# Performance work log

Hardware: AMD Instinct MI355X
Metric: run time of the kernel (lower is better)

The kernel has to match this reference:

```python
import jax, jax.numpy as jnp
import numpy as np

HID = 2048      # hidden_size
NH = 32         # num_heads
G = 8           # num_kv_groups
R = NH // G     # repeat factor (heads per kv group)
HD = HID // NH  # head_dim = 64
SCALE = HD ** 0.5


def setup_inputs() -> dict:
    key = jax.random.key(0)
    ks = jax.random.split(key, 10)
    B, S = 2, 1024
    x = jax.random.normal(ks[0], (B, S, HID), dtype=jnp.float32)
    attention_mask = jnp.ones((B, S, S), dtype=jnp.float32)
    # Linear params stored as [in, out] (y = x @ W + b), same math as torch Linear.
    Wq = jax.random.normal(ks[1], (HID, HID), dtype=jnp.float32) * 0.02
    bq = jnp.zeros((HID,), dtype=jnp.float32)
    Wk = jax.random.normal(ks[2], (HID, G * HD), dtype=jnp.float32) * 0.02
    bk = jnp.zeros((G * HD,), dtype=jnp.float32)
    Wv = jax.random.normal(ks[3], (HID, G * HD), dtype=jnp.float32) * 0.02
    bv = jnp.zeros((G * HD,), dtype=jnp.float32)
    Wo = jax.random.normal(ks[4], (HID, HID), dtype=jnp.float32) * 0.02
    bo = jnp.zeros((HID,), dtype=jnp.float32)
    return {"x": x, "attention_mask": attention_mask,
            "Wq": Wq, "bq": bq, "Wk": Wk, "bk": bk,
            "Wv": Wv, "bv": bv, "Wo": Wo, "bo": bo}


def reference(x, attention_mask, Wq, bq, Wk, bk, Wv, bv, Wo, bo):
    B, S, _ = x.shape
    # Projections. Group heads as (G, R) instead of repeat_interleave:
    # repeat_interleave(key, R, dim=2) duplicates each kv group R times, which is
    # exactly sharing key[:, :, g] across the R heads of group g.
    q = (x @ Wq + bq).reshape(B, S, G, R, HD)   # [B,S,G,R,HD] (heads = G*R in order)
    k = (x @ Wk + bk).reshape(B, S, G, HD)      # [B,S,G,HD]
    v = (x @ Wv + bv).reshape(B, S, G, HD)
    # scores [B,G,R,Sq,Sk] == torch's [B, NH, Sq, Sk] with NH = G*R
    scores = jnp.einsum('bqgrd,bkgd->bgrqk', q, k) / SCALE
    scores = scores * attention_mask[:, None, None]  # multiplicative mask per head
    w = jax.nn.softmax(scores, axis=-1)
    out = jnp.einsum('bgrqk,bkgd->bqgrd', w, v).reshape(B, S, HID)
    return out @ Wo + bo + x
```

## Files before the change

### kernel.cpp

```cpp
#include <hip/hip_runtime.h>

typedef unsigned short u16;
typedef unsigned int u32;
typedef __attribute__((ext_vector_type(8))) short bf16x8;
typedef __attribute__((ext_vector_type(4))) float f32x4;

#define HID 2048
#define S_LEN 1024
#define BATCH 2
#define G_KV 8
#define R_REP 4
#define HD 64
#define NQKV 3072

__device__ __forceinline__ u16 f2bf(float f) {
    union { u32 u; float ff; } x; x.ff = f;
    u32 u = x.u;
    u += 0x7FFFu + ((u >> 16) & 1u);
    return (u16)(u >> 16);
}

__device__ __forceinline__ void gload_lds16(const void* g, void* l) {
    __builtin_amdgcn_global_load_lds((const __attribute__((address_space(1))) void*)g,
                                     (__attribute__((address_space(3))) void*)l,
                                     16, 0, 0);
}

__global__ __launch_bounds__(256) void cvt_x(const float* __restrict__ in,
                                             u16* __restrict__ out) {
    int i = (blockIdx.x * 256 + threadIdx.x) * 8;
    float4 a = *(const float4*)(in + i);
    float4 b = *(const float4*)(in + i + 4);
    u16 t[8] = {f2bf(a.x), f2bf(a.y), f2bf(a.z), f2bf(a.w),
                f2bf(b.x), f2bf(b.y), f2bf(b.z), f2bf(b.w)};
    *(uint4*)(out + i) = *(const uint4*)t;
}

__global__ __launch_bounds__(256) void mask_perm(const float* __restrict__ mask,
                                                 float* __restrict__ out) {
    __shared__ float tile[64 * 68];
    int bid = blockIdx.x;
    int kt = bid & 15, qblk = (bid >> 4) & 15, b = bid >> 8;
    int t = threadIdx.x;
    int row = t >> 2, c0 = (t & 3) * 16;
    const float* src = mask + ((size_t)b * S_LEN + qblk * 64 + row) * S_LEN + kt * 64 + c0;
#pragma unroll
    for (int i = 0; i < 4; ++i)
        *(float4*)&tile[row * 68 + c0 + i * 4] = *(const float4*)(src + i * 4);
    __syncthreads();
    int w = t >> 6, quad = (t >> 4) & 3, l16 = t & 15;
    int q = w * 16 + l16;
    float* dst = out + (size_t)bid * 4096 + t * 16;
#pragma unroll
    for (int mt = 0; mt < 4; ++mt) {
        float4 v = *(const float4*)&tile[q * 68 + mt * 16 + quad * 4];
        *(float4*)(dst + mt * 4) = v;
    }
}

__global__ __launch_bounds__(256) void transpose_qkv(const float* __restrict__ Wq,
                                                     const float* __restrict__ Wk,
                                                     const float* __restrict__ Wv,
                                                     u16* __restrict__ out) {
    __shared__ float tile[32][33];
    int n0 = blockIdx.x * 32, k0 = blockIdx.y * 32;
    const float* in; int N, nc0;
    if (n0 < 2048)      { in = Wq; N = 2048; nc0 = n0; }
    else if (n0 < 2560) { in = Wk; N = 512;  nc0 = n0 - 2048; }
    else                { in = Wv; N = 512;  nc0 = n0 - 2560; }
    int tx = threadIdx.x, ty = threadIdx.y;
#pragma unroll
    for (int j = 0; j < 4; ++j)
        tile[ty + j * 8][tx] = in[(size_t)(k0 + ty + j * 8) * N + nc0 + tx];
    __syncthreads();
#pragma unroll
    for (int j = 0; j < 4; ++j)
        out[(size_t)(n0 + ty + j * 8) * 2048 + k0 + tx] = f2bf(tile[tx][ty + j * 8]);
}

__global__ __launch_bounds__(256) void transpose_cvt(const float* __restrict__ in,
                                                     u16* __restrict__ out,
                                                     int K, int N) {
    __shared__ float tile[32][33];
    int n0 = blockIdx.x * 32, k0 = blockIdx.y * 32;
    int tx = threadIdx.x, ty = threadIdx.y;
#pragma unroll
    for (int j = 0; j < 4; ++j)
        tile[ty + j * 8][tx] = in[(size_t)(k0 + ty + j * 8) * N + n0 + tx];
    __syncthreads();
#pragma unroll
    for (int j = 0; j < 4; ++j)
        out[(size_t)(n0 + ty + j * 8) * K + k0 + tx] = f2bf(tile[tx][ty + j * 8]);
}

__global__ __launch_bounds__(256) void gemm_qkv(const u16* __restrict__ Xb,
                                                const u16* __restrict__ WT,
                                                const float* __restrict__ bq,
                                                const float* __restrict__ bk,
                                                const float* __restrict__ bv,
                                                u16* __restrict__ qb,
                                                u16* __restrict__ kb,
                                                u16* __restrict__ vb) {
    __shared__ __align__(16) u16 As[64 * 32];
    __shared__ __align__(16) u16 Bs[128 * 32];
    int tid = threadIdx.x;
    int w = tid >> 6, lane = tid & 63, quad = lane >> 4, l16 = lane & 15;
    int m0 = blockIdx.y * 64, n0 = blockIdx.x * 128;
    int wr = (w >> 1) * 32, wc = (w & 1) * 64;
    int srow = lane >> 2, scol = (lane & 3) * 8;

    f32x4 acc[2][4];
#pragma unroll
    for (int i = 0; i < 2; ++i)
#pragma unroll
        for (int j = 0; j < 4; ++j) acc[i][j] = (f32x4){0.f, 0.f, 0.f, 0.f};

    for (int k0 = 0; k0 < 2048; k0 += 32) {
        gload_lds16(&Xb[(size_t)(m0 + w * 16 + srow) * 2048 + k0 + scol], &As[(w * 16) * 32]);
#pragma unroll
        for (int c = 0; c < 2; ++c) {
            int row = w * 32 + c * 16;
            gload_lds16(&WT[(size_t)(n0 + row + srow) * 2048 + k0 + scol], &Bs[row * 32]);
        }
        __syncthreads();
        bf16x8 af[2], bfr[4];
#pragma unroll
        for (int mt = 0; mt < 2; ++mt)
            af[mt] = *(const bf16x8*)&As[(wr + mt * 16 + l16) * 32 + quad * 8];
#pragma unroll
        for (int nt = 0; nt < 4; ++nt)
            bfr[nt] = *(const bf16x8*)&Bs[(wc + nt * 16 + l16) * 32 + quad * 8];
#pragma unroll
        for (int mt = 0; mt < 2; ++mt)
#pragma unroll
            for (int nt = 0; nt < 4; ++nt)
                acc[mt][nt] = __builtin_amdgcn_mfma_f32_16x16x32_bf16(af[mt], bfr[nt], acc[mt][nt], 0, 0, 0);
        __syncthreads();
    }

#pragma unroll
    for (int nt = 0; nt < 4; ++nt) {
        int n = n0 + wc + nt * 16 + l16;
        float bias;
        if (n < 2048) bias = bq[n];
        else if (n < 2560) bias = bk[n - 2048];
        else bias = bv[n - 2560];
#pragma unroll
        for (int mt = 0; mt < 2; ++mt) {
#pragma unroll
            for (int reg = 0; reg < 4; ++reg) {
                int m = m0 + wr + mt * 16 + quad * 4 + reg;
                float val = acc[mt][nt][reg] + bias;
                int b = m >> 10, s = m & 1023;
                if (n < 2048) {
                    int g = n >> 8, r = (n >> 6) & 3, d = n & 63;
                    qb[((((size_t)(b * G_KV + g) * R_REP + r) * S_LEN) + s) * HD + d] = f2bf(val * 0.125f);
                } else if (n < 2560) {
                    int n2 = n - 2048, g = n2 >> 6, d = n2 & 63;
                    kb[(((size_t)(b * G_KV + g) * S_LEN) + s) * HD + d] = f2bf(val);
                } else {
                    int n2 = n - 2560, g = n2 >> 6, d = n2 & 63;
                    vb[(((size_t)(b * G_KV + g) * HD + d) * S_LEN) + s] = f2bf(val);
                }
            }
        }
    }
}

__global__ __launch_bounds__(256) void attn_mfma(const u16* __restrict__ qbuf,
                                                 const u16* __restrict__ kbuf,
                                                 const u16* __restrict__ vtbuf,
                                                 const float* __restrict__ mask_pm,
                                                 u16* __restrict__ aout) {
    __shared__ __align__(16) u16 Ks[64 * 72];
    __shared__ __align__(16) u16 Vs[64 * 72];
    __shared__ __align__(16) u16 Ps[64 * 72];
    __shared__ float l_lds[64];

    int d = blockIdx.x;
    int xcd = d & 7, j = d >> 3;
    int pr = xcd * 2 + (j >> 6);
    int r = (j >> 4) & 3, qblk = j & 15;
    int b = pr >> 3, g = pr & 7;

    int tid = threadIdx.x;
    int w = tid >> 6, lane = tid & 63, quad = lane >> 4, l16 = lane & 15;
    int s0 = qblk * 64;
    int q = w * 16 + l16;

    const u16* qrow = qbuf +
        ((((size_t)(b * G_KV + g) * R_REP + r) * S_LEN) + s0 + q) * HD;
    bf16x8 qf0 = *(const bf16x8*)(qrow + quad * 8);
    bf16x8 qf1 = *(const bf16x8*)(qrow + 32 + quad * 8);

    f32x4 o_acc[4];
#pragma unroll
    for (int i = 0; i < 4; ++i) o_acc[i] = (f32x4){0.f, 0.f, 0.f, 0.f};
    float l_part = 0.f;

    const u16* kbase  = kbuf  + (size_t)(b * G_KV + g) * S_LEN * HD;
    const u16* vtbase = vtbuf + (size_t)(b * G_KV + g) * HD * S_LEN;
    const float* mbase = mask_pm + ((size_t)(b * 16 + qblk) * 16) * 4096 + tid * 16;

    int srow = tid >> 2, sc = (tid & 3) * 16;

    uint4 kp0, kp1, vp0, vp1;
    f32x4 mc[4], mn[4];
    {
        const u16* kr = kbase + (size_t)srow * HD + sc;
        kp0 = *(const uint4*)kr; kp1 = *(const uint4*)(kr + 8);
        const u16* vr = vtbase + (size_t)srow * S_LEN + sc;
        vp0 = *(const uint4*)vr; vp1 = *(const uint4*)(vr + 8);
#pragma unroll
        for (int i = 0; i < 4; ++i) mc[i] = *(const f32x4*)(mbase + i * 4);
    }

    for (int kt = 0; kt < 16; ++kt) {
        __syncthreads();
        *(uint4*)&Ks[srow * 72 + sc]     = kp0;
        *(uint4*)&Ks[srow * 72 + sc + 8] = kp1;
        *(uint4*)&Vs[srow * 72 + sc]     = vp0;
        *(uint4*)&Vs[srow * 72 + sc + 8] = vp1;
        __syncthreads();

        if (kt < 15) {
            int nk = (kt + 1) * 64;
            const u16* kr = kbase + (size_t)(nk + srow) * HD + sc;
            kp0 = *(const uint4*)kr; kp1 = *(const uint4*)(kr + 8);
            const u16* vr = vtbase + (size_t)srow * S_LEN + nk + sc;
            vp0 = *(const uint4*)vr; vp1 = *(const uint4*)(vr + 8);
            const float* mr = mbase + (size_t)(kt + 1) * 4096;
#pragma unroll
            for (int i = 0; i < 4; ++i) mn[i] = *(const f32x4*)(mr + i * 4);
        }

#pragma unroll
        for (int mt = 0; mt < 4; ++mt) {
            bf16x8 af0 = *(const bf16x8*)&Ks[(mt * 16 + l16) * 72 + quad * 8];
            bf16x8 af1 = *(const bf16x8*)&Ks[(mt * 16 + l16) * 72 + 32 + quad * 8];
            f32x4 z = (f32x4){0.f, 0.f, 0.f, 0.f};
            z = __builtin_amdgcn_mfma_f32_16x16x32_bf16(af0, qf0, z, 0, 0, 0);
            f32x4 s = __builtin_amdgcn_mfma_f32_16x16x32_bf16(af1, qf1, s = z, 0, 0, 0);

            u32 er[4];
#pragma unroll
            for (int rg = 0; rg < 4; ++rg) {
                float e = __expf(s[rg] * mc[mt][rg]);
                u32 u = __float_as_uint(e) + 0x8000u;
                er[rg] = u;
                l_part += __uint_as_float(u & 0xFFFF0000u);
            }
            uint2 pk;
            pk.x = __builtin_amdgcn_perm(er[1], er[0], 0x07060302u);
            pk.y = __builtin_amdgcn_perm(er[3], er[2], 0x07060302u);
            *(uint2*)&Ps[q * 72 + mt * 16 + quad * 4] = pk;
        }

        bf16x8 pf0 = *(const bf16x8*)&Ps[q * 72 + quad * 8];
        bf16x8 pf1 = *(const bf16x8*)&Ps[q * 72 + 32 + quad * 8];
#pragma unroll
        for (int nt = 0; nt < 4; ++nt) {
            bf16x8 vf0 = *(const bf16x8*)&Vs[(nt * 16 + l16) * 72 + quad * 8];
            bf16x8 vf1 = *(const bf16x8*)&Vs[(nt * 16 + l16) * 72 + 32 + quad * 8];
            o_acc[nt] = __builtin_amdgcn_mfma_f32_16x16x32_bf16(pf0, vf0, o_acc[nt], 0, 0, 0);
            o_acc[nt] = __builtin_amdgcn_mfma_f32_16x16x32_bf16(pf1, vf1, o_acc[nt], 0, 0, 0);
        }
#pragma unroll
        for (int i = 0; i < 4; ++i) mc[i] = mn[i];
    }

    l_part += __shfl_xor(l_part, 16);
    l_part += __shfl_xor(l_part, 32);
    l_lds[w * 16 + l16] = l_part;

#pragma unroll
    for (int reg = 0; reg < 4; ++reg) {
        int row = w * 16 + quad * 4 + reg;
        float inv = 1.0f / l_lds[row];
        int sidx = s0 + row;
        u16* dst = aout + ((size_t)(b * S_LEN + sidx)) * HID + (g * R_REP + r) * HD;
#pragma unroll
        for (int nt = 0; nt < 4; ++nt)
            dst[nt * 16 + l16] = f2bf(o_acc[nt][reg] * inv);
    }
}

__global__ __launch_bounds__(256) void gemm_o(const u16* __restrict__ A,
                                              const u16* __restrict__ WT,
                                              const float* __restrict__ bo,
                                              const float* __restrict__ Xres,
                                              float* __restrict__ out) {
    __shared__ __align__(16) u16 As[64 * 32];
    __shared__ __align__(16) u16 Bs[128 * 32];
    int tid = threadIdx.x;
    int w = tid >> 6, lane = tid & 63, quad = lane >> 4, l16 = lane & 15;
    int m0 = blockIdx.y * 64, n0 = blockIdx.x * 128;
    int wr = (w >> 1) * 32, wc = (w & 1) * 64;
    int srow = lane >> 2, scol = (lane & 3) * 8;

    f32x4 acc[2][4];
#pragma unroll
    for (int i = 0; i < 2; ++i)
#pragma unroll
        for (int j = 0; j < 4; ++j) acc[i][j] = (f32x4){0.f, 0.f, 0.f, 0.f};

    for (int k0 = 0; k0 < 2048; k0 += 32) {
        gload_lds16(&A[(size_t)(m0 + w * 16 + srow) * 2048 + k0 + scol], &As[(w * 16) * 32]);
#pragma unroll
        for (int c = 0; c < 2; ++c) {
            int row = w * 32 + c * 16;
            gload_lds16(&WT[(size_t)(n0 + row + srow) * 2048 + k0 + scol], &Bs[row * 32]);
        }
        __syncthreads();
        bf16x8 af[2], bfr[4];
#pragma unroll
        for (int mt = 0; mt < 2; ++mt)
            af[mt] = *(const bf16x8*)&As[(wr + mt * 16 + l16) * 32 + quad * 8];
#pragma unroll
        for (int nt = 0; nt < 4; ++nt)
            bfr[nt] = *(const bf16x8*)&Bs[(wc + nt * 16 + l16) * 32 + quad * 8];
#pragma unroll
        for (int mt = 0; mt < 2; ++mt)
#pragma unroll
            for (int nt = 0; nt < 4; ++nt)
                acc[mt][nt] = __builtin_amdgcn_mfma_f32_16x16x32_bf16(af[mt], bfr[nt], acc[mt][nt], 0, 0, 0);
        __syncthreads();
    }

#pragma unroll
    for (int nt = 0; nt < 4; ++nt) {
        int n = n0 + wc + nt * 16 + l16;
        float bias = bo[n];
#pragma unroll
        for (int mt = 0; mt < 2; ++mt) {
#pragma unroll
            for (int reg = 0; reg < 4; ++reg) {
                int m = m0 + wr + mt * 16 + quad * 4 + reg;
                out[(size_t)m * 2048 + n] = acc[mt][nt][reg] + bias + Xres[(size_t)m * 2048 + n];
            }
        }
    }
}

extern "C" void kernel_launch(void* const* d_in, const int* in_sizes, int n_in,
                              void* d_out, int out_size, void* d_ws, size_t ws_size,
                              hipStream_t stream) {
    const float* x    = (const float*)d_in[0];
    const float* mask = (const float*)d_in[1];
    const float* Wq   = (const float*)d_in[2];
    const float* bq   = (const float*)d_in[3];
    const float* Wk   = (const float*)d_in[4];
    const float* bk   = (const float*)d_in[5];
    const float* Wv   = (const float*)d_in[6];
    const float* bv   = (const float*)d_in[7];
    const float* Wo   = (const float*)d_in[8];
    const float* bo   = (const float*)d_in[9];
    float* out = (float*)d_out;

    u16* ws = (u16*)d_ws;
    size_t off = 0;
    u16* WqkvT = ws + off; off += (size_t)NQKV * 2048;
    u16* WoT   = ws + off; off += (size_t)2048 * 2048;
    u16* q_buf = ws + off; off += (size_t)BATCH * G_KV * R_REP * S_LEN * HD;
    u16* k_buf = ws + off; off += (size_t)BATCH * G_KV * S_LEN * HD;
    u16* v_buf = ws + off; off += (size_t)BATCH * G_KV * S_LEN * HD;
    u16* a_out = ws + off; off += (size_t)2048 * 2048;
    u16* Xb       = a_out;
    float* mask_pm = (float*)WqkvT;

    cvt_x<<<dim3(2048 * 2048 / (256 * 8)), 256, 0, stream>>>(x, Xb);

    dim3 tb(32, 8);
    transpose_qkv<<<dim3(96, 64), tb, 0, stream>>>(Wq, Wk, Wv, WqkvT);
    transpose_cvt<<<dim3(64, 64), tb, 0, stream>>>(Wo, WoT, 2048, 2048);

    gemm_qkv<<<dim3(NQKV / 128, 2048 / 64), 256, 0, stream>>>(Xb, WqkvT, bq, bk, bv,
                                                              q_buf, k_buf, v_buf);

    mask_perm<<<dim3(BATCH * 16 * 16), 256, 0, stream>>>(mask, mask_pm);

    attn_mfma<<<dim3(BATCH * G_KV * R_REP * (S_LEN / 64)), 256, 0, stream>>>(
        q_buf, k_buf, v_buf, mask_pm, a_out);

    gemm_o<<<dim3(2048 / 128, 2048 / 64), 256, 0, stream>>>(a_out, WoT, bo, x, out);
}
```

Before: 242.6 us.

## Add 4-stage LDS software pipeline to QKV and output projection GEMMs

Both projection GEMMs now keep four LDS buffers, prefetch three k-tiles ahead with direct global-to-LDS loads, and use a partial vmcnt wait plus a single barrier per iteration instead of two __syncthreads. The goal is to hide global memory latency behind the MFMA work, which the old load-sync-compute-sync loop exposed every step. In exchange LDS use per block grows fourfold, which may lower occupancy. Correctness relies on the hand-counted vmcnt value and on the buffer-reuse distance.

```diff
diff --git a/kernel.cpp b/kernel.cpp
--- a/kernel.cpp
+++ b/kernel.cpp
@@ -101,42 +101,63 @@
                                                 u16* __restrict__ qb,
                                                 u16* __restrict__ kb,
                                                 u16* __restrict__ vb) {
-    __shared__ __align__(16) u16 As[64 * 32];
-    __shared__ __align__(16) u16 Bs[128 * 32];
+    __shared__ __align__(16) u16 As[4][64 * 32];
+    __shared__ __align__(16) u16 Bs[4][128 * 32];
     int tid = threadIdx.x;
     int w = tid >> 6, lane = tid & 63, quad = lane >> 4, l16 = lane & 15;
     int m0 = blockIdx.y * 64, n0 = blockIdx.x * 128;
     int wr = (w >> 1) * 32, wc = (w & 1) * 64;
     int srow = lane >> 2, scol = (lane & 3) * 8;
 
+    const u16* aP  = &Xb[(size_t)(m0 + w * 16 + srow) * 2048 + scol];
+    const u16* bP0 = &WT[(size_t)(n0 + w * 32 + srow) * 2048 + scol];
+    const u16* bP1 = &WT[(size_t)(n0 + w * 32 + 16 + srow) * 2048 + scol];
+    u16* aL  = &As[0][(w * 16) * 32];
+    u16* bL0 = &Bs[0][(w * 32) * 32];
+    u16* bL1 = &Bs[0][(w * 32 + 16) * 32];
+
     f32x4 acc[2][4];
 #pragma unroll
     for (int i = 0; i < 2; ++i)
 #pragma unroll
         for (int j = 0; j < 4; ++j) acc[i][j] = (f32x4){0.f, 0.f, 0.f, 0.f};
 
-    for (int k0 = 0; k0 < 2048; k0 += 32) {
-        gload_lds16(&Xb[(size_t)(m0 + w * 16 + srow) * 2048 + k0 + scol], &As[(w * 16) * 32]);
-#pragma unroll
-        for (int c = 0; c < 2; ++c) {
-            int row = w * 32 + c * 16;
-            gload_lds16(&WT[(size_t)(n0 + row + srow) * 2048 + k0 + scol], &Bs[row * 32]);
-        }
-        __syncthreads();
+#pragma unroll
+    for (int p = 0; p < 3; ++p) {
+        int ko = p * 32;
+        gload_lds16(aP + ko,  aL  + p * (64 * 32));
+        gload_lds16(bP0 + ko, bL0 + p * (128 * 32));
+        gload_lds16(bP1 + ko, bL1 + p * (128 * 32));
+    }
+
+#pragma unroll 4
+    for (int t = 0; t < 64; ++t) {
+        asm volatile("s_waitcnt vmcnt(6)" ::: "memory");
+        __builtin_amdgcn_s_barrier();
+        __builtin_amdgcn_sched_barrier(0);
+
+        int tn = t + 3;
+        int ko = (tn < 64 ? tn : 63) * 32;
+        int bn = tn & 3;
+        gload_lds16(aP + ko,  aL  + bn * (64 * 32));
+        gload_lds16(bP0 + ko, bL0 + bn * (128 * 32));
+        gload_lds16(bP1 + ko, bL1 + bn * (128 * 32));
+
+        int cb = t & 3;
         bf16x8 af[2], bfr[4];
 #pragma unroll
         for (int mt = 0; mt < 2; ++mt)
-            af[mt] = *(const bf16x8*)&As[(wr + mt * 16 + l16) * 32 + quad * 8];
+            af[mt] = *(const bf16x8*)&As[cb][(wr + mt * 16 + l16) * 32 + quad * 8];
 #pragma unroll
         for (int nt = 0; nt < 4; ++nt)
-            bfr[nt] = *(const bf16x8*)&Bs[(wc + nt * 16 + l16) * 32 + quad * 8];
+            bfr[nt] = *(const bf16x8*)&Bs[cb][(wc + nt * 16 + l16) * 32 + quad * 8];
 #pragma unroll
         for (int mt = 0; mt < 2; ++mt)
 #pragma unroll
             for (int nt = 0; nt < 4; ++nt)
                 acc[mt][nt] = __builtin_amdgcn_mfma_f32_16x16x32_bf16(af[mt], bfr[nt], acc[mt][nt], 0, 0, 0);
-        __syncthreads();
-    }
+    }
+    asm volatile("s_waitcnt vmcnt(0)" ::: "memory");
 
 #pragma unroll
     for (int nt = 0; nt < 4; ++nt) {
@@ -290,42 +311,63 @@
                                               const float* __restrict__ bo,
                                               const float* __restrict__ Xres,
                                               float* __restrict__ out) {
-    __shared__ __align__(16) u16 As[64 * 32];
-    __shared__ __align__(16) u16 Bs[128 * 32];
+    __shared__ __align__(16) u16 As[4][64 * 32];
+    __shared__ __align__(16) u16 Bs[4][128 * 32];
     int tid = threadIdx.x;
     int w = tid >> 6, lane = tid & 63, quad = lane >> 4, l16 = lane & 15;
     int m0 = blockIdx.y * 64, n0 = blockIdx.x * 128;
     int wr = (w >> 1) * 32, wc = (w & 1) * 64;
     int srow = lane >> 2, scol = (lane & 3) * 8;
 
+    const u16* aP  = &A[(size_t)(m0 + w * 16 + srow) * 2048 + scol];
+    const u16* bP0 = &WT[(size_t)(n0 + w * 32 + srow) * 2048 + scol];
+    const u16* bP1 = &WT[(size_t)(n0 + w * 32 + 16 + srow) * 2048 + scol];
+    u16* aL  = &As[0][(w * 16) * 32];
+    u16* bL0 = &Bs[0][(w * 32) * 32];
+    u16* bL1 = &Bs[0][(w * 32 + 16) * 32];
+
     f32x4 acc[2][4];
 #pragma unroll
     for (int i = 0; i < 2; ++i)
 #pragma unroll
         for (int j = 0; j < 4; ++j) acc[i][j] = (f32x4){0.f, 0.f, 0.f, 0.f};
 
-    for (int k0 = 0; k0 < 2048; k0 += 32) {
-        gload_lds16(&A[(size_t)(m0 + w * 16 + srow) * 2048 + k0 + scol], &As[(w * 16) * 32]);
-#pragma unroll
-        for (int c = 0; c < 2; ++c) {
-            int row = w * 32 + c * 16;
-            gload_lds16(&WT[(size_t)(n0 + row + srow) * 2048 + k0 + scol], &Bs[row * 32]);
-        }
-        __syncthreads();
+#pragma unroll
+    for (int p = 0; p < 3; ++p) {
+        int ko = p * 32;
+        gload_lds16(aP + ko,  aL  + p * (64 * 32));
+        gload_lds16(bP0 + ko, bL0 + p * (128 * 32));
+        gload_lds16(bP1 + ko, bL1 + p * (128 * 32));
+    }
+
+#pragma unroll 4
+    for (int t = 0; t < 64; ++t) {
+        asm volatile("s_waitcnt vmcnt(6)" ::: "memory");
+        __builtin_amdgcn_s_barrier();
+        __builtin_amdgcn_sched_barrier(0);
+
+        int tn = t + 3;
+        int ko = (tn < 64 ? tn : 63) * 32;
+        int bn = tn & 3;
+        gload_lds16(aP + ko,  aL  + bn * (64 * 32));
+        gload_lds16(bP0 + ko, bL0 + bn * (128 * 32));
+        gload_lds16(bP1 + ko, bL1 + bn * (128 * 32));
+
+        int cb = t & 3;
         bf16x8 af[2], bfr[4];
 #pragma unroll
         for (int mt = 0; mt < 2; ++mt)
-            af[mt] = *(const bf16x8*)&As[(wr + mt * 16 + l16) * 32 + quad * 8];
+            af[mt] = *(const bf16x8*)&As[cb][(wr + mt * 16 + l16) * 32 + quad * 8];
 #pragma unroll
         for (int nt = 0; nt < 4; ++nt)
-            bfr[nt] = *(const bf16x8*)&Bs[(wc + nt * 16 + l16) * 32 + quad * 8];
+            bfr[nt] = *(const bf16x8*)&Bs[cb][(wc + nt * 16 + l16) * 32 + quad * 8];
 #pragma unroll
         for (int mt = 0; mt < 2; ++mt)
 #pragma unroll
             for (int nt = 0; nt < 4; ++nt)
                 acc[mt][nt] = __builtin_amdgcn_mfma_f32_16x16x32_bf16(af[mt], bfr[nt], acc[mt][nt], 0, 0, 0);
-        __syncthreads();
-    }
+    }
+    asm volatile("s_waitcnt vmcnt(0)" ::: "memory");
 
 #pragma unroll
     for (int nt = 0; nt < 4; ++nt) {
```

Measured after the change: 246.2 us. About the same (+1.5%).
